# Kernel tuning notes

Hardware: AMD Instinct MI355X
Metric: run time of the kernel (lower is better)

The kernel has to match this reference:

```python
import math
import jax, jax.numpy as jnp
import numpy as np

B, S, HIDDEN = 1, 4096, 2048
HEADS, KVH = 16, 4
HD = HIDDEN // HEADS            # 128
GROUPS = HEADS // KVH           # 4
CHUNK = 1024                    # ring_attention_chunk_size
BASE = 500000.0
MAXPOS = 131072
ORIG = 8192
BFAST, BSLOW, MSCALE_CFG = 32.0, 1.0, 1.0
SCALING = MAXPOS / ORIG


def _yarn_inv_freq():
    dim = HD
    pos_freqs = BASE ** (np.arange(0, dim, 2, dtype=np.float32) / dim)
    extrap = 1.0 / pos_freqs
    interp = 1.0 / (SCALING * pos_freqs)
    low = max(math.floor(dim * math.log(ORIG / (BFAST * 2 * math.pi)) / (2 * math.log(BASE))), 0)
    high = min(math.ceil(dim * math.log(ORIG / (BSLOW * 2 * math.pi)) / (2 * math.log(BASE))), dim - 1)
    i = np.arange(dim // 2, dtype=np.float32)
    smooth = np.clip((i - low) / max(high - low, 1), 0.0, 1.0)  # i<low -> interp, i>high -> extrap
    inv = (1.0 - smooth) * interp + smooth * extrap
    return jnp.asarray(inv, jnp.float32)

INV_FREQ = _yarn_inv_freq()
MSCALE = (0.1 * math.log(SCALING) + 1.0) * MSCALE_CFG  # scaling > 1


def rotate_half(x):
    x1, x2 = jnp.split(x, 2, axis=-1)
    return jnp.concatenate((-x2, x1), axis=-1)


def ring_attention(q, k, v, chunk, causal=True):
    # q,k,v: [B,H,S,D]; kv_len divisible by chunk
    b, h, s, d = q.shape
    kv_len = k.shape[2]
    nc = kv_len // chunk
    scale = d ** (-0.5)
    k_chunks = jnp.moveaxis(k.reshape(b, h, nc, chunk, d), 2, 0)  # [nc,B,H,chunk,D]
    v_chunks = jnp.moveaxis(v.reshape(b, h, nc, chunk, d), 2, 0)
    kv_starts = jnp.arange(nc) * chunk
    q_idx = jnp.arange(s)[:, None]
    k_off = jnp.arange(chunk)[None, :]
    neg_inf = jnp.float32(-jnp.inf)

    def step(carry, inp):
        out, mx, se = carry
        kch, vch, kv_start = inp
        scores = jnp.einsum('bhqd,bhkd->bhqk', q, kch) * scale
        if causal:
            mask = (kv_start + k_off) > q_idx  # [S, chunk]
            scores = jnp.where(mask[None, None], neg_inf, scores)
        chunk_max = scores.max(axis=-1, keepdims=True)
        new_max = jnp.maximum(mx, chunk_max)
        exp_old = se * jnp.exp(mx - new_max)
        exp_chunk = jnp.exp(scores - new_max)
        exp_sum_chunk = exp_chunk.sum(axis=-1, keepdims=True)
        denom = exp_old + exp_sum_chunk + 1e-10
        out = out * (se / denom) + jnp.einsum('bhqk,bhkd->bhqd', exp_chunk, vch) / denom
        return (out, new_max, exp_old + exp_sum_chunk), None

    init = (jnp.zeros_like(q),
            jnp.full((b, h, s, 1), -jnp.inf, dtype=q.dtype),
            jnp.zeros((b, h, s, 1), dtype=q.dtype))
    (out, _, _), _ = jax.lax.scan(step, init, (k_chunks, v_chunks, kv_starts))
    return out


def setup_inputs() -> dict:
    key = jax.random.key(0)
    ks = jax.random.split(key, 5)
    hidden_states = jax.random.normal(ks[0], (B, S, HIDDEN), dtype=jnp.float32)
    position_ids = jnp.broadcast_to(jnp.arange(S, dtype=jnp.int32)[None, :], (B, S))
    sd = 1.0 / math.sqrt(HIDDEN)
    Wq = jax.random.normal(ks[1], (HIDDEN, HEADS * HD), dtype=jnp.float32) * sd
    Wk = jax.random.normal(ks[2], (HIDDEN, KVH * HD), dtype=jnp.float32) * sd
    Wv = jax.random.normal(ks[3], (HIDDEN, KVH * HD), dtype=jnp.float32) * sd
    Wo = jax.random.normal(ks[4], (HEADS * HD, HIDDEN), dtype=jnp.float32) * sd
    return {'hidden_states': hidden_states, 'position_ids': position_ids,
            'Wq': Wq, 'Wk': Wk, 'Wv': Wv, 'Wo': Wo}


def reference(hidden_states, position_ids, Wq, Wk, Wv, Wo):
    b, s, _ = hidden_states.shape
    q = (hidden_states @ Wq).reshape(b, s, HEADS, HD).transpose(0, 2, 1, 3)
    k = (hidden_states @ Wk).reshape(b, s, KVH, HD).transpose(0, 2, 1, 3)
    v = (hidden_states @ Wv).reshape(b, s, KVH, HD).transpose(0, 2, 1, 3)
    # YaRN rope
    freqs = position_ids.astype(jnp.float32)[:, :, None] * INV_FREQ[None, None, :]  # [B,S,HD/2]
    emb = jnp.concatenate((freqs, freqs), axis=-1)  # [B,S,HD]
    cos = (jnp.cos(emb) * MSCALE)[:, None]  # [B,1,S,HD]
    sin = (jnp.sin(emb) * MSCALE)[:, None]
    q = q * cos + rotate_half(q) * sin
    k = k * cos + rotate_half(k) * sin
    # GQA expand
    k = jnp.repeat(k, GROUPS, axis=1)
    v = jnp.repeat(v, GROUPS, axis=1)
    # ring path: use_ring_attention and kv_len > chunk
    attn = ring_attention(q, k, v, CHUNK, causal=True)
    attn = attn.transpose(0, 2, 1, 3).reshape(b, s, HEADS * HD)
    return attn @ Wo
```

## Files before the change

kernel.cpp:

```cpp
#include <hip/hip_runtime.h>
#include <cstdint>
#include <cstddef>


typedef unsigned short u16;
typedef unsigned int u32;
typedef float f32x4 __attribute__((ext_vector_type(4)));
typedef __bf16 bf16x8 __attribute__((ext_vector_type(8)));

__device__ __forceinline__ u16 f2bf(float f) {
    union { float f; u32 u; } v; v.f = f;
    u32 u = v.u;
    u += 0x7fffu + ((u >> 16) & 1u);
    return (u16)(u >> 16);
}
__device__ __forceinline__ float bf2f(u16 b) {
    union { u32 u; float f; } v; v.u = ((u32)b) << 16;
    return v.f;
}
__device__ __forceinline__ u16 f2h(float f) {
    union { _Float16 h; u16 u; } v; v.h = (_Float16)f; return v.u;
}
__device__ __forceinline__ float h2f(u16 u) {
    union { u16 u; _Float16 h; } v; v.u = u; return (float)v.h;
}

__device__ __forceinline__ void load16_to_lds(const void* g, void* l) {
    __builtin_amdgcn_global_load_lds((const __attribute__((address_space(1))) u32*)g,
                                     (__attribute__((address_space(3))) u32*)l,
                                     16, 0, 0);
}

#define MFMA16(a, b, c) __builtin_amdgcn_mfma_f32_16x16x32_bf16((a), (b), (c), 0, 0, 0)

__global__ __launch_bounds__(256) void convert_f32_bf16(const float* __restrict__ X,
                                                        u16* __restrict__ Y) {
    const int i = (blockIdx.x * 256 + threadIdx.x) * 4;
    const float4 v = *(const float4*)(X + i);
    union { u16 s[4]; uint2 u; } pk;
    pk.s[0] = f2bf(v.x); pk.s[1] = f2bf(v.y); pk.s[2] = f2bf(v.z); pk.s[3] = f2bf(v.w);
    *(uint2*)(Y + i) = pk.u;
}

__global__ __launch_bounds__(256) void transpose_w(const float* __restrict__ W,
                                                   u16* __restrict__ Wt, int N) {
    __shared__ float tile[64][65];
    const int n0 = blockIdx.x * 64, k0 = blockIdx.y * 64;
    const int tc = threadIdx.x & 63, tr = threadIdx.x >> 6;
#pragma unroll
    for (int i = 0; i < 64; i += 4)
        tile[tc][tr + i] = W[(size_t)(k0 + tr + i) * N + n0 + tc];
    __syncthreads();
#pragma unroll
    for (int i = 0; i < 64; i += 4)
        Wt[(size_t)(n0 + tr + i) * 2048 + k0 + tc] = f2bf(tile[tr + i][tc]);
}

__device__ __forceinline__ void store_out(float* p, float v) { *p = v; }
__device__ __forceinline__ void store_out(u16* p, float v) { *p = f2bf(v); }

template <typename OutT>
__global__ __launch_bounds__(256) void gemm_bt(const u16* __restrict__ A,
                                               const u16* __restrict__ Bt,
                                               OutT* __restrict__ C,
                                               int M, int N, int K) {
    __shared__ __align__(16) u16 sA[8192];
    __shared__ __align__(16) u16 sB[8192];
    const int t = threadIdx.x;
    const int lane = t & 63, w = t >> 6;
    const int quad = lane >> 4, l15 = lane & 15;
    const int m0 = blockIdx.x << 7, n0 = blockIdx.y << 7;
    const int wr4 = (w >> 1) * 4, wc4 = (w & 1) * 4;
    f32x4 acc[4][4] = {};
    for (int k0 = 0; k0 < K; k0 += 64) {
        __syncthreads();
#pragma unroll
        for (int r = 0; r < 2; ++r) {
            const int f = w * 2 + r;
#pragma unroll
            for (int kc = 0; kc < 2; ++kc) {
                load16_to_lds(A + (size_t)(m0 + f * 16 + l15) * K + k0 + kc * 32 + quad * 8,
                              sA + (f * 2 + kc) * 512);
                load16_to_lds(Bt + (size_t)(n0 + f * 16 + l15) * K + k0 + kc * 32 + quad * 8,
                              sB + (f * 2 + kc) * 512);
            }
        }
        __syncthreads();
#pragma unroll
        for (int kc = 0; kc < 2; ++kc) {
            bf16x8 af[4], bb[4];
#pragma unroll
            for (int i = 0; i < 4; ++i)
                af[i] = *(const bf16x8*)(sA + ((wr4 + i) * 2 + kc) * 512 + lane * 8);
#pragma unroll
            for (int j = 0; j < 4; ++j)
                bb[j] = *(const bf16x8*)(sB + ((wc4 + j) * 2 + kc) * 512 + lane * 8);
#pragma unroll
            for (int i = 0; i < 4; ++i)
#pragma unroll
                for (int j = 0; j < 4; ++j)
                    acc[i][j] = MFMA16(af[i], bb[j], acc[i][j]);
        }
    }
#pragma unroll
    for (int i = 0; i < 4; ++i)
#pragma unroll
        for (int j = 0; j < 4; ++j) {
            const int row = m0 + (w >> 1) * 64 + i * 16 + quad * 4;
            const int col = n0 + (w & 1) * 64 + j * 16 + l15;
#pragma unroll
            for (int r = 0; r < 4; ++r)
                store_out(C + (size_t)(row + r) * N + col, acc[i][j][r]);
        }
}

__global__ __launch_bounds__(256) void rope_kernel(u16* __restrict__ QKV,
                                                   const int* __restrict__ pos_ids) {
    const int idx = blockIdx.x * 256 + threadIdx.x;
    const int NQ = 4096 * 16 * 64;
    u16* p;
    int s, i;
    if (idx < NQ) {
        s = idx >> 10;
        const int hi = idx & 1023;
        const int h = hi >> 6;
        i = hi & 63;
        p = QKV + (size_t)s * 3072 + h * 128 + i;
    } else {
        const int k = idx - NQ;
        if (k >= 4096 * 4 * 64) return;
        s = k >> 8;
        const int hi = k & 255;
        const int h = hi >> 6;
        i = hi & 63;
        p = QKV + (size_t)s * 3072 + 2048 + h * 128 + i;
    }
    const float pf = (float)pos_ids[s];
    const float fi = (float)i;
    const float pos_freq = powf(500000.0f, fi * (1.0f / 64.0f));
    const float inv_ex = 1.0f / pos_freq;
    const float inv_in = inv_ex * (1.0f / 16.0f);
    const float sm = fminf(fmaxf((fi - 18.0f) * (1.0f / 17.0f), 0.0f), 1.0f);
    const float inv = (1.0f - sm) * inv_in + sm * inv_ex;
    const float ph = pf * inv;
    const float MS = 1.2772588722239781f;
    const float cs = cosf(ph) * MS, sn = sinf(ph) * MS;
    const float x1 = bf2f(p[0]), x2 = bf2f(p[64]);
    p[0] = f2bf(x1 * cs - x2 * sn);
    p[64] = f2bf(x2 * cs + x1 * sn);
}

__global__ __launch_bounds__(256) void transpose_v(const u16* __restrict__ QKV,
                                                   u16* __restrict__ Vt) {
    __shared__ u16 tile[64 * 72];
    const int t = threadIdx.x;
    const int k0 = blockIdx.x * 64, d0 = blockIdx.y * 64, kvh = blockIdx.z;
#pragma unroll
    for (int k = 0; k < 4; ++k) {
        const int u = t + k * 256;
        const int key = u >> 4, dg = u & 15;
        const uint2 v = *(const uint2*)(QKV + (size_t)(k0 + key) * 3072 + 2560 + kvh * 128 + d0 + dg * 4);
        *(uint2*)(tile + key * 72 + dg * 4) = v;
    }
    __syncthreads();
#pragma unroll
    for (int k = 0; k < 4; ++k) {
        const int u = t + k * 256;
        const int d = u >> 4, kg = u & 15;
        union { u16 s[4]; uint2 v; } pk;
#pragma unroll
        for (int i = 0; i < 4; ++i) pk.s[i] = tile[(kg * 4 + i) * 72 + d];
        *(uint2*)(Vt + (size_t)(kvh * 128 + d0 + d) * 4096 + k0 + kg * 4) = pk.v;
    }
}

__global__ __launch_bounds__(256, 2) void attn_partial(const u16* __restrict__ QKV,
                                                       const u16* __restrict__ Vt,
                                                       u16* __restrict__ part,
                                                       float* __restrict__ ml) {
    __shared__ __align__(16) u16 sK[8192];
    __shared__ __align__(16) u16 sV[8192];
    __shared__ __align__(16) u16 sP[8192];

    const int t = threadIdx.x;
    const int lane = t & 63, w = t >> 6;
    const int quad = lane >> 4, l15 = lane & 15;
    const int bid = blockIdx.x;
    const int u = bid >> 4, h = bid & 15, kvh = h >> 2;

    int qb, c;
    if (u < 8)       { qb = 8 + u; c = 0; }
    else if (u < 24) { const int r = u - 8;  qb = 16 + (r >> 1); c = r & 1; }
    else if (u < 48) { const int r = u - 24; const int q3 = r / 3; qb = 24 + q3; c = r - q3 * 3; }
    else             { const int r = u - 48; const int k = r >> 2; const int g0 = r & 3;
                       qb = g0 * 8 + (7 - k); c = g0; }
    const int g = qb >> 3;
    const int q0 = qb << 7, kv0 = c << 10;
    const int jmax = (c == g) ? (2 * (qb & 7) + 2) : 16;

    {
        u16* dst0 = (w < 2) ? (u16*)sK : (u16*)sV;
        const int fbase = (w & 1) * 8;
#pragma unroll
        for (int idx = 0; idx < 8; ++idx) {
            const int qg = idx >> 2, kc = idx & 3;
            load16_to_lds(QKV + (size_t)(q0 + w * 32 + qg * 16 + l15) * 3072 + h * 128 + kc * 32 + quad * 8,
                          dst0 + (fbase + idx) * 512);
        }
    }
    __syncthreads();
    bf16x8 af[2][4];
    {
        const u16* src0 = (w < 2) ? (const u16*)sK : (const u16*)sV;
        const int fbase = (w & 1) * 8;
#pragma unroll
        for (int qg = 0; qg < 2; ++qg)
#pragma unroll
            for (int kc = 0; kc < 4; ++kc)
                af[qg][kc] = *(const bf16x8*)(src0 + (fbase + qg * 4 + kc) * 512 + lane * 8);
    }

    float m_c[2] = {-1e30f, -1e30f}, l_c[2] = {0.0f, 0.0f};
    f32x4 o_c[8][2] = {};
    const float SCALE = 0.08838834764831845f;

    for (int j = 0; j < jmax; ++j) {
        const int kt0 = kv0 + (j << 6);
        __syncthreads();
        {
            const u16* gk = QKV + (size_t)(kt0 + w * 16 + l15) * 3072 + 2048 + kvh * 128 + quad * 8;
#pragma unroll
            for (int kc = 0; kc < 4; ++kc)
                load16_to_lds(gk + kc * 32, sK + (w * 4 + kc) * 512);
#pragma unroll
            for (int r = 0; r < 4; ++r) {
                const int dt = w * 2 + (r >> 1), ks = r & 1;
                load16_to_lds(Vt + (size_t)(kvh * 128 + dt * 16 + l15) * 4096 + kt0 + ks * 32 + quad * 8,
                              sV + (dt * 2 + ks) * 512);
            }
        }
        __syncthreads();

        f32x4 sacc[4][2] = {};
#pragma unroll
        for (int j4 = 0; j4 < 4; ++j4)
#pragma unroll
            for (int kc = 0; kc < 4; ++kc) {
                const bf16x8 kf = *(const bf16x8*)(sK + (j4 * 4 + kc) * 512 + lane * 8);
                sacc[j4][0] = MFMA16(kf, af[0][kc], sacc[j4][0]);
                sacc[j4][1] = MFMA16(kf, af[1][kc], sacc[j4][1]);
            }

        const bool diag = (c == g) && ((j >> 1) == (qb & 7));
        if (diag) {
#pragma unroll
            for (int j4 = 0; j4 < 4; ++j4)
#pragma unroll
                for (int qg = 0; qg < 2; ++qg) {
                    const int qrow = q0 + w * 32 + qg * 16 + l15;
#pragma unroll
                    for (int r = 0; r < 4; ++r) {
                        const int key = kt0 + j4 * 16 + quad * 4 + r;
                        sacc[j4][qg][r] = (key > qrow) ? -1e30f : sacc[j4][qg][r] * SCALE;
                    }
                }
        } else {
#pragma unroll
            for (int j4 = 0; j4 < 4; ++j4)
#pragma unroll
                for (int qg = 0; qg < 2; ++qg)
#pragma unroll
                    for (int r = 0; r < 4; ++r)
                        sacc[j4][qg][r] *= SCALE;
        }

#pragma unroll
        for (int qg = 0; qg < 2; ++qg) {
            float mx = -1e30f;
#pragma unroll
            for (int j4 = 0; j4 < 4; ++j4)
#pragma unroll
                for (int r = 0; r < 4; ++r) mx = fmaxf(mx, sacc[j4][qg][r]);
            mx = fmaxf(mx, __shfl_xor(mx, 16, 64));
            mx = fmaxf(mx, __shfl_xor(mx, 32, 64));
            const float mn = fmaxf(m_c[qg], mx);
            const float alpha = __expf(m_c[qg] - mn);
            float ps = 0.0f;
#pragma unroll
            for (int j4 = 0; j4 < 4; ++j4)
#pragma unroll
                for (int r = 0; r < 4; ++r) {
                    const float pe = __expf(sacc[j4][qg][r] - mn);
                    sacc[j4][qg][r] = pe;
                    ps += pe;
                }
            ps += __shfl_xor(ps, 16, 64);
            ps += __shfl_xor(ps, 32, 64);
            l_c[qg] = l_c[qg] * alpha + ps;
            m_c[qg] = mn;
#pragma unroll
            for (int dt = 0; dt < 8; ++dt) o_c[dt][qg] *= alpha;
        }

#pragma unroll
        for (int ks = 0; ks < 2; ++ks)
#pragma unroll
            for (int jj = 0; jj < 2; ++jj) {
                const int j4 = ks * 2 + jj;
                const int quadp = jj * 2 + (quad >> 1);
#pragma unroll
                for (int qg = 0; qg < 2; ++qg)
#pragma unroll
                    for (int pr = 0; pr < 2; ++pr) {
                        const int r = pr * 2;
                        const int jje = (quad & 1) * 4 + r;
                        const u32 pk = ((u32)f2bf(sacc[j4][qg][r + 1]) << 16) | f2bf(sacc[j4][qg][r]);
                        *(u32*)(sP + w * 2048 + (qg * 2 + ks) * 512 + (quadp * 16 + l15) * 8 + jje) = pk;
                    }
            }

#pragma unroll
        for (int ks = 0; ks < 2; ++ks) {
            const bf16x8 pf0 = *(const bf16x8*)(sP + w * 2048 + (0 * 2 + ks) * 512 + lane * 8);
            const bf16x8 pf1 = *(const bf16x8*)(sP + w * 2048 + (1 * 2 + ks) * 512 + lane * 8);
#pragma unroll
            for (int dt = 0; dt < 8; ++dt) {
                const bf16x8 vf = *(const bf16x8*)(sV + (dt * 2 + ks) * 512 + lane * 8);
                o_c[dt][0] = MFMA16(vf, pf0, o_c[dt][0]);
                o_c[dt][1] = MFMA16(vf, pf1, o_c[dt][1]);
            }
        }
    }

#pragma unroll
    for (int qg = 0; qg < 2; ++qg) {
        const float invl = 1.0f / l_c[qg];
        const int q = w * 32 + qg * 16 + l15;
#pragma unroll
        for (int dt = 0; dt < 8; ++dt)
#pragma unroll
            for (int r = 0; r < 4; ++r)
                part[(size_t)bid * 16384 + (dt * 16 + quad * 4 + r) * 128 + q] =
                    f2h(o_c[dt][qg][r] * invl);
        if (quad == 0) {
            ml[(size_t)bid * 256 + q * 2] = m_c[qg];
            ml[(size_t)bid * 256 + q * 2 + 1] = l_c[qg];
        }
    }
}

__global__ __launch_bounds__(256) void attn_merge(const u16* __restrict__ part,
                                                  const float* __restrict__ ml,
                                                  u16* __restrict__ attn) {
    const int b = blockIdx.x;
    const int qb = b >> 4, h = b & 15;
    const int g = qb >> 3;
    const int t = threadIdx.x;
    const int qrow = t & 127;
    const int d0 = blockIdx.y * 64 + (t >> 7) * 32;

    float o[32];
#pragma unroll
    for (int i = 0; i < 32; ++i) o[i] = 0.0f;
    float m_g = -1e30f, l_g = 0.0f;

    for (int c = 0; c <= g; ++c) {
        int u;
        if (c == g)      u = 48 + (7 - (qb & 7)) * 4 + g;
        else if (g == 1) u = qb - 8;
        else if (g == 2) u = 8 + (qb - 16) * 2 + c;
        else             u = 24 + (qb - 24) * 3 + c;
        const int tile = u * 16 + h;
        const float m_c = ml[(size_t)tile * 256 + qrow * 2];
        const float l_c = ml[(size_t)tile * 256 + qrow * 2 + 1];
        const float mn = fmaxf(m_g, m_c);
        const float a = l_g * __expf(m_g - mn);
        const float eC = __expf(m_c - mn);
        const float sE = l_c * eC;
        const float d = a + sE + 1e-10f;
        const float f_old = l_g / d;
        const float f_new = sE / d;
#pragma unroll
        for (int i = 0; i < 32; ++i) {
            const float v = h2f(part[(size_t)tile * 16384 + (d0 + i) * 128 + qrow]);
            o[i] = o[i] * f_old + v * f_new;
        }
        l_g = a + sE;
        m_g = mn;
    }

    u16* dst = attn + (size_t)(qb * 128 + qrow) * 2048 + h * 128 + d0;
#pragma unroll
    for (int kq = 0; kq < 4; ++kq) {
        union { u16 s[8]; uint4 v; } pk;
#pragma unroll
        for (int i = 0; i < 8; ++i) pk.s[i] = f2bf(o[kq * 8 + i]);
        *(uint4*)(dst + kq * 8) = pk.v;
    }
}

extern "C" void kernel_launch(void* const* d_in, const int* in_sizes, int n_in,
                              void* d_out, int out_size, void* d_ws, size_t ws_size,
                              hipStream_t stream) {
    const float* X  = (const float*)d_in[0];
    const int* pos  = (const int*)d_in[1];
    const float* Wq = (const float*)d_in[2];
    const float* Wk = (const float*)d_in[3];
    const float* Wv = (const float*)d_in[4];
    const float* Wo = (const float*)d_in[5];
    float* out = (float*)d_out;
    char* ws = (char*)d_ws;

    u16*   part = (u16*)(ws);
    u16*   Xbf  = (u16*)(ws);
    u16*   Wt   = (u16*)(ws + 16777216);
    u16*   QKV  = (u16*)(ws + 41943040);
    u16*   attn = (u16*)(ws + 41943040);
    u16*   Vt   = (u16*)(ws + 67108864);
    float* ml   = (float*)(ws + 71303168);
    u16*   Wot  = (u16*)(ws + 72613888);

    convert_f32_bf16<<<8192, 256, 0, stream>>>(X, Xbf);
    transpose_w<<<dim3(32, 32), 256, 0, stream>>>(Wq, Wt, 2048);
    transpose_w<<<dim3(8, 32), 256, 0, stream>>>(Wk, Wt + (size_t)2048 * 2048, 512);
    transpose_w<<<dim3(8, 32), 256, 0, stream>>>(Wv, Wt + (size_t)2560 * 2048, 512);
    transpose_w<<<dim3(32, 32), 256, 0, stream>>>(Wo, Wot, 2048);

    gemm_bt<u16><<<dim3(32, 24), 256, 0, stream>>>(Xbf, Wt, QKV, 4096, 3072, 2048);

    rope_kernel<<<20480, 256, 0, stream>>>(QKV, pos);
    transpose_v<<<dim3(64, 2, 4), 256, 0, stream>>>(QKV, Vt);

    attn_partial<<<1280, 256, 0, stream>>>(QKV, Vt, part, ml);
    attn_merge<<<dim3(512, 2), 256, 0, stream>>>(part, ml, attn);

    gemm_bt<float><<<dim3(32, 16), 256, 0, stream>>>(attn, Wot, out, 4096, 2048, 2048);
}
```

Measured before the change: 459.2 us.

## Double-buffer K/V tiles in attention and merge preprocessing kernel launches

The attention kernel now double-buffers its K and V LDS tiles, so the asynchronous global-to-LDS load of the next 64-key tile is issued while the current tile is being computed, and one barrier per iteration is dropped. The four weight-transpose launches are merged into one grid, and RoPE and the V transpose are fused into a single launch. The convert kernel now handles four float4s per thread. The extra LDS buffers raise shared-memory use per block, which may reduce occupancy of the attention kernel.

```diff
diff --git a/kernel.cpp b/kernel.cpp
--- a/kernel.cpp
+++ b/kernel.cpp
@@ -35,17 +35,31 @@
 
 __global__ __launch_bounds__(256) void convert_f32_bf16(const float* __restrict__ X,
                                                         u16* __restrict__ Y) {
-    const int i = (blockIdx.x * 256 + threadIdx.x) * 4;
-    const float4 v = *(const float4*)(X + i);
-    union { u16 s[4]; uint2 u; } pk;
-    pk.s[0] = f2bf(v.x); pk.s[1] = f2bf(v.y); pk.s[2] = f2bf(v.z); pk.s[3] = f2bf(v.w);
-    *(uint2*)(Y + i) = pk.u;
-}
-
-__global__ __launch_bounds__(256) void transpose_w(const float* __restrict__ W,
-                                                   u16* __restrict__ Wt, int N) {
+    const int base = (blockIdx.x * 1024 + threadIdx.x) * 4;
+#pragma unroll
+    for (int k = 0; k < 4; ++k) {
+        const int i = base + k * 1024;
+        const float4 v = *(const float4*)(X + i);
+        union { u16 s[4]; uint2 u; } pk;
+        pk.s[0] = f2bf(v.x); pk.s[1] = f2bf(v.y); pk.s[2] = f2bf(v.z); pk.s[3] = f2bf(v.w);
+        *(uint2*)(Y + i) = pk.u;
+    }
+}
+
+__global__ __launch_bounds__(256) void transpose_w4(const float* __restrict__ Wq,
+                                                    const float* __restrict__ Wk,
+                                                    const float* __restrict__ Wv,
+                                                    const float* __restrict__ Wo,
+                                                    u16* __restrict__ Wt,
+                                                    u16* __restrict__ Wot) {
     __shared__ float tile[64][65];
-    const int n0 = blockIdx.x * 64, k0 = blockIdx.y * 64;
+    const int bx = blockIdx.x;
+    const float* W; u16* dst; int N, n0;
+    if (bx < 32)      { W = Wq; dst = Wt;                          N = 2048; n0 = bx * 64; }
+    else if (bx < 40) { W = Wk; dst = Wt + (size_t)2048 * 2048;    N = 512;  n0 = (bx - 32) * 64; }
+    else if (bx < 48) { W = Wv; dst = Wt + (size_t)2560 * 2048;    N = 512;  n0 = (bx - 40) * 64; }
+    else              { W = Wo; dst = Wot;                         N = 2048; n0 = (bx - 48) * 64; }
+    const int k0 = blockIdx.y * 64;
     const int tc = threadIdx.x & 63, tr = threadIdx.x >> 6;
 #pragma unroll
     for (int i = 0; i < 64; i += 4)
@@ -53,7 +67,7 @@
     __syncthreads();
 #pragma unroll
     for (int i = 0; i < 64; i += 4)
-        Wt[(size_t)(n0 + tr + i) * 2048 + k0 + tc] = f2bf(tile[tr + i][tc]);
+        dst[(size_t)(n0 + tr + i) * 2048 + k0 + tc] = f2bf(tile[tr + i][tc]);
 }
 
 __device__ __forceinline__ void store_out(float* p, float v) { *p = v; }
@@ -114,8 +128,33 @@
         }
 }
 
-__global__ __launch_bounds__(256) void rope_kernel(u16* __restrict__ QKV,
-                                                   const int* __restrict__ pos_ids) {
+__global__ __launch_bounds__(256) void rope_vt_kernel(u16* __restrict__ QKV,
+                                                      u16* __restrict__ Vt,
+                                                      const int* __restrict__ pos_ids) {
+    __shared__ u16 tile[64 * 72];
+    if (blockIdx.x >= 20480) {
+        const int b = blockIdx.x - 20480;
+        const int k0 = (b & 63) * 64, d0 = ((b >> 6) & 1) * 64, kvh = b >> 7;
+        const int t = threadIdx.x;
+#pragma unroll
+        for (int k = 0; k < 4; ++k) {
+            const int u = t + k * 256;
+            const int key = u >> 4, dg = u & 15;
+            const uint2 v = *(const uint2*)(QKV + (size_t)(k0 + key) * 3072 + 2560 + kvh * 128 + d0 + dg * 4);
+            *(uint2*)(tile + key * 72 + dg * 4) = v;
+        }
+        __syncthreads();
+#pragma unroll
+        for (int k = 0; k < 4; ++k) {
+            const int u = t + k * 256;
+            const int d = u >> 4, kg = u & 15;
+            union { u16 s[4]; uint2 v; } pk;
+#pragma unroll
+            for (int i = 0; i < 4; ++i) pk.s[i] = tile[(kg * 4 + i) * 72 + d];
+            *(uint2*)(Vt + (size_t)(kvh * 128 + d0 + d) * 4096 + k0 + kg * 4) = pk.v;
+        }
+        return;
+    }
     const int idx = blockIdx.x * 256 + threadIdx.x;
     const int NQ = 4096 * 16 * 64;
     u16* p;
@@ -128,7 +167,6 @@
         p = QKV + (size_t)s * 3072 + h * 128 + i;
     } else {
         const int k = idx - NQ;
-        if (k >= 4096 * 4 * 64) return;
         s = k >> 8;
         const int hi = k & 255;
         const int h = hi >> 6;
@@ -150,27 +188,19 @@
     p[64] = f2bf(x2 * cs + x1 * sn);
 }
 
-__global__ __launch_bounds__(256) void transpose_v(const u16* __restrict__ QKV,
-                                                   u16* __restrict__ Vt) {
-    __shared__ u16 tile[64 * 72];
-    const int t = threadIdx.x;
-    const int k0 = blockIdx.x * 64, d0 = blockIdx.y * 64, kvh = blockIdx.z;
-#pragma unroll
-    for (int k = 0; k < 4; ++k) {
-        const int u = t + k * 256;
-        const int key = u >> 4, dg = u & 15;
-        const uint2 v = *(const uint2*)(QKV + (size_t)(k0 + key) * 3072 + 2560 + kvh * 128 + d0 + dg * 4);
-        *(uint2*)(tile + key * 72 + dg * 4) = v;
-    }
-    __syncthreads();
-#pragma unroll
-    for (int k = 0; k < 4; ++k) {
-        const int u = t + k * 256;
-        const int d = u >> 4, kg = u & 15;
-        union { u16 s[4]; uint2 v; } pk;
-#pragma unroll
-        for (int i = 0; i < 4; ++i) pk.s[i] = tile[(kg * 4 + i) * 72 + d];
-        *(uint2*)(Vt + (size_t)(kvh * 128 + d0 + d) * 4096 + k0 + kg * 4) = pk.v;
+__device__ __forceinline__ void stage_kv(const u16* __restrict__ QKV,
+                                         const u16* __restrict__ Vt,
+                                         int kt0, int kvh, int w, int l15, int quad,
+                                         u16* bK, u16* bV) {
+    const u16* gk = QKV + (size_t)(kt0 + w * 16 + l15) * 3072 + 2048 + kvh * 128 + quad * 8;
+#pragma unroll
+    for (int kc = 0; kc < 4; ++kc)
+        load16_to_lds(gk + kc * 32, bK + (w * 4 + kc) * 512);
+#pragma unroll
+    for (int r = 0; r < 4; ++r) {
+        const int dt = w * 2 + (r >> 1), ks = r & 1;
+        load16_to_lds(Vt + (size_t)(kvh * 128 + dt * 16 + l15) * 4096 + kt0 + ks * 32 + quad * 8,
+                      bV + (dt * 2 + ks) * 512);
     }
 }
 
@@ -178,8 +208,8 @@
                                                        const u16* __restrict__ Vt,
                                                        u16* __restrict__ part,
                                                        float* __restrict__ ml) {
-    __shared__ __align__(16) u16 sK[8192];
-    __shared__ __align__(16) u16 sV[8192];
+    __shared__ __align__(16) u16 sK[2][8192];
+    __shared__ __align__(16) u16 sV[2][8192];
     __shared__ __align__(16) u16 sP[8192];
 
     const int t = threadIdx.x;
@@ -199,7 +229,7 @@
     const int jmax = (c == g) ? (2 * (qb & 7) + 2) : 16;
 
     {
-        u16* dst0 = (w < 2) ? (u16*)sK : (u16*)sV;
+        u16* dst0 = (w < 2) ? sK[0] : sK[1];
         const int fbase = (w & 1) * 8;
 #pragma unroll
         for (int idx = 0; idx < 8; ++idx) {
@@ -211,7 +241,7 @@
     __syncthreads();
     bf16x8 af[2][4];
     {
-        const u16* src0 = (w < 2) ? (const u16*)sK : (const u16*)sV;
+        const u16* src0 = (w < 2) ? sK[0] : sK[1];
         const int fbase = (w & 1) * 8;
 #pragma unroll
         for (int qg = 0; qg < 2; ++qg)
@@ -219,6 +249,9 @@
             for (int kc = 0; kc < 4; ++kc)
                 af[qg][kc] = *(const bf16x8*)(src0 + (fbase + qg * 4 + kc) * 512 + lane * 8);
     }
+    __syncthreads();
+
+    stage_kv(QKV, Vt, kv0, kvh, w, l15, quad, sK[0], sV[0]);
 
     float m_c[2] = {-1e30f, -1e30f}, l_c[2] = {0.0f, 0.0f};
     f32x4 o_c[8][2] = {};
@@ -226,27 +259,17 @@
 
     for (int j = 0; j < jmax; ++j) {
         const int kt0 = kv0 + (j << 6);
+        const int p = j & 1;
         __syncthreads();
-        {
-            const u16* gk = QKV + (size_t)(kt0 + w * 16 + l15) * 3072 + 2048 + kvh * 128 + quad * 8;
-#pragma unroll
-            for (int kc = 0; kc < 4; ++kc)
-                load16_to_lds(gk + kc * 32, sK + (w * 4 + kc) * 512);
-#pragma unroll
-            for (int r = 0; r < 4; ++r) {
-                const int dt = w * 2 + (r >> 1), ks = r & 1;
-                load16_to_lds(Vt + (size_t)(kvh * 128 + dt * 16 + l15) * 4096 + kt0 + ks * 32 + quad * 8,
-                              sV + (dt * 2 + ks) * 512);
-            }
-        }
-        __syncthreads();
+        if (j + 1 < jmax)
+            stage_kv(QKV, Vt, kv0 + ((j + 1) << 6), kvh, w, l15, quad, sK[1 - p], sV[1 - p]);
 
         f32x4 sacc[4][2] = {};
 #pragma unroll
         for (int j4 = 0; j4 < 4; ++j4)
 #pragma unroll
             for (int kc = 0; kc < 4; ++kc) {
-                const bf16x8 kf = *(const bf16x8*)(sK + (j4 * 4 + kc) * 512 + lane * 8);
+                const bf16x8 kf = *(const bf16x8*)(sK[p] + (j4 * 4 + kc) * 512 + lane * 8);
                 sacc[j4][0] = MFMA16(kf, af[0][kc], sacc[j4][0]);
                 sacc[j4][1] = MFMA16(kf, af[1][kc], sacc[j4][1]);
             }
@@ -325,7 +348,7 @@
             const bf16x8 pf1 = *(const bf16x8*)(sP + w * 2048 + (1 * 2 + ks) * 512 + lane * 8);
 #pragma unroll
             for (int dt = 0; dt < 8; ++dt) {
-                const bf16x8 vf = *(const bf16x8*)(sV + (dt * 2 + ks) * 512 + lane * 8);
+                const bf16x8 vf = *(const bf16x8*)(sV[p] + (dt * 2 + ks) * 512 + lane * 8);
                 o_c[dt][0] = MFMA16(vf, pf0, o_c[dt][0]);
                 o_c[dt][1] = MFMA16(vf, pf1, o_c[dt][1]);
             }
@@ -420,16 +443,12 @@
     float* ml   = (float*)(ws + 71303168);
     u16*   Wot  = (u16*)(ws + 72613888);
 
-    convert_f32_bf16<<<8192, 256, 0, stream>>>(X, Xbf);
-    transpose_w<<<dim3(32, 32), 256, 0, stream>>>(Wq, Wt, 2048);
-    transpose_w<<<dim3(8, 32), 256, 0, stream>>>(Wk, Wt + (size_t)2048 * 2048, 512);
-    transpose_w<<<dim3(8, 32), 256, 0, stream>>>(Wv, Wt + (size_t)2560 * 2048, 512);
-    transpose_w<<<dim3(32, 32), 256, 0, stream>>>(Wo, Wot, 2048);
+    convert_f32_bf16<<<2048, 256, 0, stream>>>(X, Xbf);
+    transpose_w4<<<dim3(80, 32), 256, 0, stream>>>(Wq, Wk, Wv, Wo, Wt, Wot);
 
     gemm_bt<u16><<<dim3(32, 24), 256, 0, stream>>>(Xbf, Wt, QKV, 4096, 3072, 2048);
 
-    rope_kernel<<<20480, 256, 0, stream>>>(QKV, pos);
-    transpose_v<<<dim3(64, 2, 4), 256, 0, stream>>>(QKV, Vt);
+    rope_vt_kernel<<<20992, 256, 0, stream>>>(QKV, Vt, pos);
 
     attn_partial<<<1280, 256, 0, stream>>>(QKV, Vt, part, ml);
     attn_merge<<<dim3(512, 2), 256, 0, stream>>>(part, ml, attn);
```

New measurement: 450.8 us. Within noise of the previous version (-1.8%).
